# Kernel optimization log

Measured on AMD Instinct MI355X. Metric: run time of the kernel, lower is better.

The kernel has to match this reference:

```python
import jax, jax.numpy as jnp
import numpy as np

B, N, C, H, MLP = 4, 1024, 768, 6, 2304  # num_heads = C // 128
D = C // H  # head dim = 128


def setup_inputs() -> dict:
    key = jax.random.key(0)
    ks = iter(jax.random.split(key, 64))
    def nrm(shape, s=0.02):
        return jax.random.normal(next(ks), shape, jnp.float32) * s
    inp = {}
    for nm in ("queries", "change_emb", "imageA_emb", "imageB_emb", "pe"):
        inp[nm] = jax.random.normal(next(ks), (B, N, C), jnp.float32)
    # three Attention modules: self-attn (1), change->ABC cross (2), imageAB->change cross (3)
    for i in (1, 2, 3):
        for p in ("q", "k", "v", "o"):
            inp[f"w{p}{i}"] = nrm((C, C))       # stored [in, out]; y = x @ W + b
            inp[f"b{p}{i}"] = jnp.zeros((C,), jnp.float32)
    for i in (1, 2, 3):
        inp[f"ln{i}_w"] = jnp.ones((C,), jnp.float32)
        inp[f"ln{i}_b"] = jnp.zeros((C,), jnp.float32)
    inp["mlp_w1"] = nrm((C, MLP)); inp["mlp_b1"] = jnp.zeros((MLP,), jnp.float32)
    inp["mlp_w2"] = nrm((MLP, C)); inp["mlp_b2"] = jnp.zeros((C,), jnp.float32)
    inp["flag_a"] = nrm((C,)); inp["flag_b"] = nrm((C,)); inp["flag_c"] = nrm((C,))
    return inp


def _ln(x, w, b, eps=1e-5):
    m = jnp.mean(x, -1, keepdims=True)
    v = jnp.var(x, -1, keepdims=True)
    return (x - m) * jax.lax.rsqrt(v + eps) * w + b


def _mha(q, k, v, wq, bq, wk, bk, wv, bv, wo, bo):
    b, nq, _ = q.shape
    qh = (q @ wq + bq).reshape(b, nq, H, D)
    kh = (k @ wk + bk).reshape(b, k.shape[1], H, D)
    vh = (v @ wv + bv).reshape(b, v.shape[1], H, D)
    scores = jnp.einsum('bqhd,bkhd->bhqk', qh, kh) / np.float32(np.sqrt(D))
    attn = jax.nn.softmax(scores, axis=-1)
    out = jnp.einsum('bhqk,bkhd->bqhd', attn, vh).reshape(b, nq, H * D)
    return out @ wo + bo


def reference(queries, change_emb, imageA_emb, imageB_emb, pe,
              wq1, bq1, wk1, bk1, wv1, bv1, wo1, bo1,
              wq2, bq2, wk2, bk2, wv2, bv2, wo2, bo2,
              wq3, bq3, wk3, bk3, wv3, bv3, wo3, bo3,
              ln1_w, ln1_b, ln2_w, ln2_b, ln3_w, ln3_b,
              mlp_w1, mlp_b1, mlp_w2, mlp_b2,
              flag_a, flag_b, flag_c):
    # --- self attention on change queries (skip_first_layer_add=False) ---
    q0 = queries + change_emb
    a = _mha(q0 + pe, q0 + pe, q0, wq1, bq1, wk1, bk1, wv1, bv1, wo1, bo1)
    q1 = _ln(q0 + a, ln1_w, ln1_b)
    # --- cross attention: change -> [imageA, imageB, change] ---
    qf = q1 + pe + flag_c
    k2 = jnp.concatenate((imageA_emb + pe + flag_a,
                          imageB_emb + pe + flag_b,
                          q1 + pe + flag_c), axis=1)
    v2 = jnp.concatenate((imageA_emb, imageB_emb, q1), axis=1)
    a = _mha(qf, k2, v2, wq2, bq2, wk2, bk2, wv2, bv2, wo2, bo2)
    q2 = _ln(q1 + a, ln2_w, ln2_b)
    # --- MLP (exact GELU, as nn.GELU default) ---
    mlp_out = jax.nn.gelu(q2 @ mlp_w1 + mlp_b1, approximate=False) @ mlp_w2 + mlp_b2
    q3 = _ln(q2 + mlp_out, ln3_w, ln3_b)
    change_out = q3
    # --- cross attention: [imageA; imageB] -> [image; change], batched along dim 0 ---
    qa = imageA_emb + pe + flag_a
    qb = imageB_emb + pe + flag_b
    ka = jnp.concatenate((imageA_emb + pe + flag_a, q3 + pe + flag_c), axis=1)
    kb = jnp.concatenate((imageB_emb + pe + flag_b, q3 + pe + flag_c), axis=1)
    va = jnp.concatenate((imageA_emb, q3), axis=1)
    vb = jnp.concatenate((imageB_emb, q3), axis=1)
    q = jnp.concatenate((qa, qb), axis=0)   # [2B, N, C]
    k = jnp.concatenate((ka, kb), axis=0)   # [2B, 2N, C]
    v = jnp.concatenate((va, vb), axis=0)
    a = _mha(q, k, v, wq3, bq3, wk3, bk3, wv3, bv3, wo3, bo3)
    q = q + a
    image_A_refined, image_B_refined = jnp.split(q, 2, axis=0)
    return (image_A_refined, image_B_refined, change_out)
```

## Files before the change

### kernel.cpp

```cpp
#include <hip/hip_runtime.h>
#include <hip/hip_bf16.h>
#include <math.h>

typedef short bf16x8 __attribute__((ext_vector_type(8)));
typedef float f32x4 __attribute__((ext_vector_type(4)));
using bf16_t = __hip_bfloat16;

#define DEV static __device__ __forceinline__

DEV unsigned short f2bu(float x) {
  bf16_t h = __float2bfloat16(x);
  unsigned short u;
  __builtin_memcpy(&u, &h, 2);
  return u;
}
DEV void st4(bf16_t* p, float a, float b, float c, float d) {
  ushort4 u;
  u.x = f2bu(a); u.y = f2bu(b); u.z = f2bu(c); u.w = f2bu(d);
  *reinterpret_cast<ushort4*>(p) = u;
}

DEV void async_copy16(const bf16_t* g, bf16_t* lds) {
  __builtin_amdgcn_global_load_lds(
      (const __attribute__((address_space(1))) unsigned int*)g,
      (__attribute__((address_space(3))) unsigned int*)lds, 16, 0, 0);
}

struct WPack {
  const float* s[12];
  bf16_t* d[12];
  float scale0;
};

__global__ __launch_bounds__(256) void k_wt12(WPack pk) {
  __shared__ float tile[32][33];
  int z = blockIdx.z;
  const float* W = pk.s[z];
  bf16_t* WT = pk.d[z];
  float scale = (z == 0) ? pk.scale0 : 1.0f;
  int i0 = blockIdx.x * 32;
  int o0 = blockIdx.y * 32;
  int tx = threadIdx.x & 31, ty = threadIdx.x >> 5;
  for (int r = ty; r < 32; r += 8)
    tile[r][tx] = W[(size_t)(i0 + r) * 768 + (o0 + tx)];
  __syncthreads();
  for (int r = ty; r < 32; r += 8)
    WT[(size_t)(o0 + r) * 768 + (i0 + tx)] = __float2bfloat16(tile[tx][r] * scale);
}

__global__ __launch_bounds__(256) void k_wt(const float* __restrict__ W, bf16_t* __restrict__ WT,
                                            int in_dim, int out_dim) {
  __shared__ float tile[32][33];
  int i0 = blockIdx.x * 32;
  int o0 = blockIdx.y * 32;
  int tx = threadIdx.x & 31, ty = threadIdx.x >> 5;
  for (int r = ty; r < 32; r += 8)
    tile[r][tx] = W[(size_t)(i0 + r) * out_dim + (o0 + tx)];
  __syncthreads();
  for (int r = ty; r < 32; r += 8)
    WT[(size_t)(o0 + r) * in_dim + (i0 + tx)] = __float2bfloat16(tile[tx][r]);
}

__global__ __launch_bounds__(256) void k_bqk(const float* __restrict__ bq, const float* __restrict__ bk,
                                             float* __restrict__ out, float qa) {
  int i = blockIdx.x * 256 + threadIdx.x;
  if (i < 768) out[i] = bq[i] * qa;
  else if (i < 1536) out[i] = bk[i - 768];
}

__global__ __launch_bounds__(256) void k_prep1(const float4* __restrict__ q, const float4* __restrict__ ce,
                                               const float4* __restrict__ pe,
                                               bf16_t* __restrict__ qpe_b, bf16_t* __restrict__ q0_b, int n4) {
  int i = blockIdx.x * 256 + threadIdx.x;
  if (i >= n4) return;
  float4 a = q[i], b = ce[i], p = pe[i];
  float sx = a.x + b.x, sy = a.y + b.y, sz = a.z + b.z, sw = a.w + b.w;
  st4(q0_b + 4 * (size_t)i, sx, sy, sz, sw);
  st4(qpe_b + 4 * (size_t)i, sx + p.x, sy + p.y, sz + p.z, sw + p.w);
}

__global__ __launch_bounds__(256) void k_addpe(const float* __restrict__ x, const float* __restrict__ pe,
                                               const float* __restrict__ flag, bf16_t* __restrict__ out) {
  int idx = blockIdx.x * 256 + threadIdx.x;
  int c = (idx % 192) * 4;
  size_t tok = (size_t)idx * 4;
  float4 xv = *(const float4*)(x + tok);
  float4 p = *(const float4*)(pe + tok);
  float4 f = *(const float4*)(flag + c);
  st4(out + tok, xv.x + p.x + f.x, xv.y + p.y + f.y, xv.z + p.z + f.z, xv.w + p.w + f.w);
}

__global__ __launch_bounds__(256) void k_buildqq(const float* __restrict__ imA, const float* __restrict__ imB,
                                                 const float* __restrict__ pe, const float* __restrict__ fa,
                                                 const float* __restrict__ fb, bf16_t* __restrict__ qq) {
  int idx = blockIdx.x * 256 + threadIdx.x;
  int c4 = idx % 192; int rem = idx / 192;
  int n = rem & 1023; int bb = rem >> 10;
  int b = bb & 3, isB = bb >> 2;
  int c = c4 * 4;
  size_t tok = (size_t)(b * 1024 + n) * 768 + c;
  float4 s = *(const float4*)((isB ? imB : imA) + tok);
  float4 p = *(const float4*)(pe + tok);
  float4 f = *(const float4*)((isB ? fb : fa) + c);
  st4(qq + (size_t)rem * 768 + c, s.x + p.x + f.x, s.y + p.y + f.y, s.z + p.z + f.z, s.w + p.w + f.w);
}

__global__ __launch_bounds__(256) void k_build2b(const float* __restrict__ q1,
    const float* __restrict__ imA, const float* __restrict__ imB, const float* __restrict__ pe,
    const float* __restrict__ fa, const float* __restrict__ fb, const float* __restrict__ fc,
    bf16_t* __restrict__ k2, bf16_t* __restrict__ v2, int b0) {
  int idx = blockIdx.x * 256 + threadIdx.x;
  int c4 = idx % 192; int rem = idx / 192;
  int bi = rem / 3072; int r3 = rem - bi * 3072;
  int seg = r3 >> 10; int n = r3 & 1023;
  int b = b0 + bi;
  int c = c4 * 4;
  size_t tok = (size_t)(b * 1024 + n) * 768 + c;
  float4 p = *(const float4*)(pe + tok);
  const float* srcp; const float* flg;
  if (seg == 0)      { srcp = imA + tok; flg = fa; }
  else if (seg == 1) { srcp = imB + tok; flg = fb; }
  else               { srcp = q1 + tok; flg = fc; }
  float4 s = *(const float4*)srcp;
  float4 f = *(const float4*)(flg + c);
  size_t o = (size_t)idx * 4;
  st4(v2 + o, s.x, s.y, s.z, s.w);
  st4(k2 + o, s.x + p.x + f.x, s.y + p.y + f.y, s.z + p.z + f.z, s.w + p.w + f.w);
}

__global__ __launch_bounds__(256) void k_build3b(const float* __restrict__ q3,
    const float* __restrict__ imA, const float* __restrict__ imB, const float* __restrict__ pe,
    const float* __restrict__ fa, const float* __restrict__ fb, const float* __restrict__ fc,
    bf16_t* __restrict__ k3, bf16_t* __restrict__ v3, int bb0) {
  int idx = blockIdx.x * 256 + threadIdx.x;
  int c4 = idx % 192; int rem = idx / 192;
  int bi = rem >> 11; int r2 = rem & 2047;
  int seg = r2 >> 10; int n = r2 & 1023;
  int bb = bb0 + bi;
  int b = bb & 3; int isB = bb >> 2;
  int c = c4 * 4;
  size_t tok = (size_t)(b * 1024 + n) * 768 + c;
  float4 p = *(const float4*)(pe + tok);
  const float* srcp; const float* flg;
  if (seg == 0) { srcp = (isB ? imB : imA) + tok; flg = isB ? fb : fa; }
  else          { srcp = q3 + tok; flg = fc; }
  float4 s = *(const float4*)srcp;
  float4 f = *(const float4*)(flg + c);
  size_t o = (size_t)idx * 4;
  st4(v3 + o, s.x, s.y, s.z, s.w);
  st4(k3 + o, s.x + p.x + f.x, s.y + p.y + f.y, s.z + p.z + f.z, s.w + p.w + f.w);
}

__global__ __launch_bounds__(256, 3) void k_flash(
    const bf16_t* __restrict__ Q, const bf16_t* __restrict__ K,
    const bf16_t* __restrict__ Vt, bf16_t* __restrict__ O,
    int Nk, int H, int ldq, int ldk, long qStrideB, long kStrideB, long oStrideB) {
  const int z = blockIdx.y; const int b = z / H, h = z % H;
  const bf16_t* Qb = Q + (size_t)b * qStrideB + h * 128;
  const bf16_t* Kb = K + (size_t)b * kStrideB + h * 128;
  const bf16_t* Vb = Vt + (size_t)z * 128 * (size_t)Nk;
  bf16_t* Ob = O + (size_t)b * oStrideB + h * 128;
  const int q0 = blockIdx.x * 64;
  const int tid = threadIdx.x, lane = tid & 63, w = tid >> 6;
  const int g = lane >> 4, c = lane & 15;

  __shared__ bf16_t Ks[64][136];
  __shared__ bf16_t Vs[128][72];
  __shared__ bf16_t Ps[64][72];

  bf16x8 qf[4];
#pragma unroll
  for (int kk = 0; kk < 4; kk++)
    qf[kk] = *reinterpret_cast<const bf16x8*>(
        &Qb[(size_t)(q0 + w * 16 + c) * ldq + kk * 32 + g * 8]);

  f32x4 oa[8];
  float m[4], l[4];
#pragma unroll
  for (int d = 0; d < 8; d++) { f32x4 zz = {0.f, 0.f, 0.f, 0.f}; oa[d] = zz; }
#pragma unroll
  for (int r = 0; r < 4; r++) { m[r] = -1.0e30f; l[r] = 0.f; }

  const int kr_ = tid >> 4, kc_ = (tid & 15) * 8;
  const int vr_ = tid >> 3, vc_ = (tid & 7) * 8;

  const int nt = Nk >> 6;
  for (int t = 0; t < nt; ++t) {
    const int k0 = t << 6;
#pragma unroll
    for (int p = 0; p < 4; p++)
      *reinterpret_cast<uint4*>(&Ks[p * 16 + kr_][kc_]) =
          *reinterpret_cast<const uint4*>(&Kb[(size_t)(k0 + p * 16 + kr_) * ldk + kc_]);
#pragma unroll
    for (int p = 0; p < 4; p++)
      *reinterpret_cast<uint4*>(&Vs[p * 32 + vr_][vc_]) =
          *reinterpret_cast<const uint4*>(&Vb[(size_t)(p * 32 + vr_) * Nk + k0 + vc_]);
    __syncthreads();

    f32x4 s[4];
#pragma unroll
    for (int j = 0; j < 4; j++) { f32x4 zz = {0.f, 0.f, 0.f, 0.f}; s[j] = zz; }
    __builtin_amdgcn_s_setprio(1);
#pragma unroll
    for (int kk = 0; kk < 4; kk++)
#pragma unroll
      for (int j = 0; j < 4; j++) {
        bf16x8 kf = *reinterpret_cast<const bf16x8*>(&Ks[j * 16 + c][kk * 32 + g * 8]);
        s[j] = __builtin_amdgcn_mfma_f32_16x16x32_bf16(qf[kk], kf, s[j], 0, 0, 0);
      }
    __builtin_amdgcn_s_setprio(0);

    float tl[4];
#pragma unroll
    for (int r = 0; r < 4; r++)
      tl[r] = fmaxf(fmaxf(s[0][r], s[1][r]), fmaxf(s[2][r], s[3][r]));
    float ex = fmaxf(fmaxf(tl[0] - m[0], tl[1] - m[1]), fmaxf(tl[2] - m[2], tl[3] - m[3]));
    if (__any(ex > 8.0f)) {
#pragma unroll
      for (int r = 0; r < 4; r++) {
        float tv = tl[r];
        tv = fmaxf(tv, __shfl_xor(tv, 1));
        tv = fmaxf(tv, __shfl_xor(tv, 2));
        tv = fmaxf(tv, __shfl_xor(tv, 4));
        tv = fmaxf(tv, __shfl_xor(tv, 8));
        float mn = fmaxf(m[r], tv);
        float f = exp2f(m[r] - mn);
        m[r] = mn;
        l[r] *= f;
#pragma unroll
        for (int d = 0; d < 8; d++) oa[d][r] *= f;
      }
    }
#pragma unroll
    for (int j = 0; j < 4; j++)
#pragma unroll
      for (int r = 0; r < 4; r++) {
        float p = exp2f(s[j][r] - m[r]);
        l[r] += p;
        Ps[w * 16 + g * 4 + r][j * 16 + c] = __float2bfloat16(p);
      }

    __builtin_amdgcn_s_setprio(1);
#pragma unroll
    for (int kk = 0; kk < 2; kk++) {
      bf16x8 pf = *reinterpret_cast<const bf16x8*>(&Ps[w * 16 + c][kk * 32 + g * 8]);
#pragma unroll
      for (int d = 0; d < 8; d++) {
        bf16x8 vf = *reinterpret_cast<const bf16x8*>(&Vs[d * 16 + c][kk * 32 + g * 8]);
        oa[d] = __builtin_amdgcn_mfma_f32_16x16x32_bf16(pf, vf, oa[d], 0, 0, 0);
      }
    }
    __builtin_amdgcn_s_setprio(0);
    __syncthreads();
  }

  float inv[4];
#pragma unroll
  for (int r = 0; r < 4; r++) {
    float t2 = l[r];
    t2 += __shfl_xor(t2, 1);
    t2 += __shfl_xor(t2, 2);
    t2 += __shfl_xor(t2, 4);
    t2 += __shfl_xor(t2, 8);
    inv[r] = 1.0f / t2;
  }
#pragma unroll
  for (int d = 0; d < 8; d++) {
    int col = d * 16 + c;
#pragma unroll
    for (int r = 0; r < 4; r++) {
      int row = q0 + w * 16 + g * 4 + r;
      Ob[(size_t)row * 768 + col] = __float2bfloat16(oa[d][r] * inv[r]);
    }
  }
}

__global__ __launch_bounds__(256) void k_ln(const float* __restrict__ X1, const float* __restrict__ X2,
                                            const float* __restrict__ A,
                                            const float* __restrict__ w, const float* __restrict__ bvec,
                                            float* __restrict__ outf, bf16_t* __restrict__ outb) {
  int row = blockIdx.x, tid = threadIdx.x;
  size_t base = (size_t)row * 768;
  float v0 = X1[base + tid] + A[base + tid];
  float v1 = X1[base + tid + 256] + A[base + tid + 256];
  float v2 = X1[base + tid + 512] + A[base + tid + 512];
  if (X2) {
    v0 += X2[base + tid]; v1 += X2[base + tid + 256]; v2 += X2[base + tid + 512];
  }
  float s = v0 + v1 + v2;
  for (int o = 32; o; o >>= 1) s += __shfl_xor(s, o);
  __shared__ float sm[8];
  int wv = tid >> 6, ln = tid & 63;
  if (ln == 0) sm[wv] = s;
  __syncthreads();
  s = sm[0] + sm[1] + sm[2] + sm[3];
  float mean = s * (1.0f / 768.0f);
  float d0 = v0 - mean, d1 = v1 - mean, d2 = v2 - mean;
  float ss = d0 * d0 + d1 * d1 + d2 * d2;
  for (int o = 32; o; o >>= 1) ss += __shfl_xor(ss, o);
  if (ln == 0) sm[4 + wv] = ss;
  __syncthreads();
  ss = sm[4] + sm[5] + sm[6] + sm[7];
  float rstd = rsqrtf(ss * (1.0f / 768.0f) + 1e-5f);
  float o0 = d0 * rstd * w[tid] + bvec[tid];
  float o1 = d1 * rstd * w[tid + 256] + bvec[tid + 256];
  float o2 = d2 * rstd * w[tid + 512] + bvec[tid + 512];
  outf[base + tid] = o0; outf[base + tid + 256] = o1; outf[base + tid + 512] = o2;
  if (outb) {
    outb[base + tid] = __float2bfloat16(o0);
    outb[base + tid + 256] = __float2bfloat16(o1);
    outb[base + tid + 512] = __float2bfloat16(o2);
  }
}

__global__ __launch_bounds__(256) void k_out3f(const float* __restrict__ imA, const float* __restrict__ imB,
                                               const float* __restrict__ pe, const float* __restrict__ fa,
                                               const float* __restrict__ fb, float* __restrict__ out) {
  int idx = blockIdx.x * 256 + threadIdx.x;
  int c4 = idx % 192; int rem = idx / 192;
  int n = rem & 1023; int bb = rem >> 10;
  int b = bb & 3, isB = bb >> 2;
  int c = c4 * 4;
  size_t tok = (size_t)(b * 1024 + n) * 768 + c;
  float4 sv = *(const float4*)((isB ? imB : imA) + tok);
  float4 p = *(const float4*)(pe + tok);
  float4 f = *(const float4*)((isB ? fb : fa) + c);
  size_t o = (size_t)idx * 4;
  float4 cur = *(float4*)(out + o);
  cur.x += sv.x + p.x + f.x;
  cur.y += sv.y + p.y + f.y;
  cur.z += sv.z + p.z + f.z;
  cur.w += sv.w + p.w + f.w;
  *(float4*)(out + o) = cur;
}

template<int OUTBF, int GELU, int OUTVT>
__global__ __launch_bounds__(256, 2) void k_gemm(
    const bf16_t* __restrict__ X, const bf16_t* __restrict__ Wt,
    const float* __restrict__ bias, void* __restrict__ Out,
    int M, int Nout, int K, int ldx, int ldw, int ldo, float alpha, int vNk) {
  const int brow = blockIdx.y * 128;
  const int bcol = blockIdx.x * 128;

  __shared__ bf16_t As[128 * 32];
  __shared__ bf16_t Bs[128 * 32];

  const int tid = threadIdx.x;
  const int lane = tid & 63;
  const int wave = tid >> 6;
  const int wr = wave >> 1;
  const int wc = wave & 1;

  f32x4 acc[4][4];
#pragma unroll
  for (int i = 0; i < 4; i++)
#pragma unroll
    for (int j = 0; j < 4; j++) {
      f32x4 zz = {0.f, 0.f, 0.f, 0.f};
      acc[i][j] = zz;
    }

  const int sr = lane >> 2;
  const int sc = (lane & 3) * 8;
  const int lrow = lane & 15;
  const int kch = (lane >> 4) * 8;

  const int nK = K >> 5;
  for (int kk = 0; kk < nK; ++kk) {
    const int k0 = kk << 5;
#pragma unroll
    for (int q = 0; q < 2; q++) {
      const int rows = wave * 32 + q * 16;
      async_copy16(X + (size_t)(brow + rows + sr) * ldx + k0 + sc, As + rows * 32);
      async_copy16(Wt + (size_t)(bcol + rows + sr) * ldw + k0 + sc, Bs + rows * 32);
    }
    __syncthreads();

    bf16x8 afr[4], bfr[4];
#pragma unroll
    for (int i = 0; i < 4; i++)
      afr[i] = *reinterpret_cast<const bf16x8*>(&As[(wr * 64 + i * 16 + lrow) * 32 + kch]);
#pragma unroll
    for (int j = 0; j < 4; j++)
      bfr[j] = *reinterpret_cast<const bf16x8*>(&Bs[(wc * 64 + j * 16 + lrow) * 32 + kch]);
#pragma unroll
    for (int i = 0; i < 4; i++)
#pragma unroll
      for (int j = 0; j < 4; j++)
        acc[i][j] = __builtin_amdgcn_mfma_f32_16x16x32_bf16(afr[i], bfr[j], acc[i][j], 0, 0, 0);
    __syncthreads();
  }

  const int lcol = lane & 15;
  const int lrow4 = (lane >> 4) * 4;

  if (OUTVT) {
    const int bi = brow / vNk;
    const int n0 = brow - bi * vNk;
#pragma unroll
    for (int i = 0; i < 4; i++) {
      int rloc = n0 + wr * 64 + i * 16 + lrow4;
#pragma unroll
      for (int j = 0; j < 4; j++) {
        int col = bcol + wc * 64 + j * 16 + lcol;
        int hh = col >> 7, dd = col & 127;
        float bv = bias ? bias[col] : 0.0f;
        ushort4 u;
        u.x = f2bu((acc[i][j][0] + bv) * alpha);
        u.y = f2bu((acc[i][j][1] + bv) * alpha);
        u.z = f2bu((acc[i][j][2] + bv) * alpha);
        u.w = f2bu((acc[i][j][3] + bv) * alpha);
        bf16_t* dst = reinterpret_cast<bf16_t*>(Out) +
                      ((size_t)(bi * 6 + hh) * 128 + dd) * (size_t)vNk + rloc;
        *reinterpret_cast<ushort4*>(dst) = u;
      }
    }
    return;
  }

#pragma unroll
  for (int i = 0; i < 4; i++) {
    int row0 = brow + wr * 64 + i * 16 + lrow4;
#pragma unroll
    for (int j = 0; j < 4; j++) {
      int col = bcol + wc * 64 + j * 16 + lcol;
      float bv = bias ? bias[col] : 0.0f;
#pragma unroll
      for (int r = 0; r < 4; r++) {
        float v = (acc[i][j][r] + bv) * alpha;
        if (GELU) v = 0.5f * v * (1.0f + erff(v * 0.70710678118f));
        size_t idx = (size_t)(row0 + r) * ldo + col;
        if (OUTBF) reinterpret_cast<bf16_t*>(Out)[idx] = __float2bfloat16(v);
        else reinterpret_cast<float*>(Out)[idx] = v;
      }
    }
  }
}

struct GArgs {
  const bf16_t* X; const bf16_t* Wt; const float* bias; bf16_t* Out;
  int K, ldx, ldw, ldo, vNk, mode;
};

__global__ __launch_bounds__(256, 2) void k_gemmD(GArgs a0, GArgs a1, int cnt0, int nx0, int nx1) {
  GArgs a; int bx, by;
  {
    int idx = blockIdx.x;
    if (idx < cnt0) { a = a0; bx = idx % nx0; by = idx / nx0; }
    else { idx -= cnt0; a = a1; bx = idx % nx1; by = idx / nx1; }
  }
  const int brow = by * 128;
  const int bcol = bx * 128;

  __shared__ bf16_t As[128 * 32];
  __shared__ bf16_t Bs[128 * 32];

  const int tid = threadIdx.x;
  const int lane = tid & 63;
  const int wave = tid >> 6;
  const int wr = wave >> 1;
  const int wc = wave & 1;

  f32x4 acc[4][4];
#pragma unroll
  for (int i = 0; i < 4; i++)
#pragma unroll
    for (int j = 0; j < 4; j++) {
      f32x4 zz = {0.f, 0.f, 0.f, 0.f};
      acc[i][j] = zz;
    }

  const int sr = lane >> 2;
  const int sc = (lane & 3) * 8;
  const int lrow = lane & 15;
  const int kch = (lane >> 4) * 8;

  const int nK = a.K >> 5;
  for (int kk = 0; kk < nK; ++kk) {
    const int k0 = kk << 5;
#pragma unroll
    for (int q = 0; q < 2; q++) {
      const int rows = wave * 32 + q * 16;
      async_copy16(a.X + (size_t)(brow + rows + sr) * a.ldx + k0 + sc, As + rows * 32);
      async_copy16(a.Wt + (size_t)(bcol + rows + sr) * a.ldw + k0 + sc, Bs + rows * 32);
    }
    __syncthreads();

    bf16x8 afr[4], bfr[4];
#pragma unroll
    for (int i = 0; i < 4; i++)
      afr[i] = *reinterpret_cast<const bf16x8*>(&As[(wr * 64 + i * 16 + lrow) * 32 + kch]);
#pragma unroll
    for (int j = 0; j < 4; j++)
      bfr[j] = *reinterpret_cast<const bf16x8*>(&Bs[(wc * 64 + j * 16 + lrow) * 32 + kch]);
#pragma unroll
    for (int i = 0; i < 4; i++)
#pragma unroll
      for (int j = 0; j < 4; j++)
        acc[i][j] = __builtin_amdgcn_mfma_f32_16x16x32_bf16(afr[i], bfr[j], acc[i][j], 0, 0, 0);
    __syncthreads();
  }

  const int lcol = lane & 15;
  const int lrow4 = (lane >> 4) * 4;

  if (a.mode == 2) {
    const int bi = brow / a.vNk;
    const int n0 = brow - bi * a.vNk;
#pragma unroll
    for (int i = 0; i < 4; i++) {
      int rloc = n0 + wr * 64 + i * 16 + lrow4;
#pragma unroll
      for (int j = 0; j < 4; j++) {
        int col = bcol + wc * 64 + j * 16 + lcol;
        int hh = col >> 7, dd = col & 127;
        float bv = a.bias[col];
        ushort4 u;
        u.x = f2bu(acc[i][j][0] + bv);
        u.y = f2bu(acc[i][j][1] + bv);
        u.z = f2bu(acc[i][j][2] + bv);
        u.w = f2bu(acc[i][j][3] + bv);
        bf16_t* dst = a.Out + ((size_t)(bi * 6 + hh) * 128 + dd) * (size_t)a.vNk + rloc;
        *reinterpret_cast<ushort4*>(dst) = u;
      }
    }
  } else {
#pragma unroll
    for (int i = 0; i < 4; i++) {
      int row0 = brow + wr * 64 + i * 16 + lrow4;
#pragma unroll
      for (int j = 0; j < 4; j++) {
        int col = bcol + wc * 64 + j * 16 + lcol;
        float bv = a.bias[col];
#pragma unroll
        for (int r = 0; r < 4; r++)
          a.Out[(size_t)(row0 + r) * a.ldo + col] = __float2bfloat16(acc[i][j][r] + bv);
      }
    }
  }
}

static inline void gemm(hipStream_t st, const bf16_t* X, const bf16_t* Wt, const float* bias,
                        void* out, int outBf, int gelu, int M, int N, int K,
                        int ldx, int ldw, int ldo, float alpha = 1.0f, int vtNk = 0) {
  dim3 g(N / 128, M / 128), blk(256);
  if (vtNk) {
    k_gemm<1, 0, 1><<<g, blk, 0, st>>>(X, Wt, bias, out, M, N, K, ldx, ldw, ldo, alpha, vtNk);
  } else if (outBf) {
    if (gelu) k_gemm<1, 1, 0><<<g, blk, 0, st>>>(X, Wt, bias, out, M, N, K, ldx, ldw, ldo, alpha, 0);
    else      k_gemm<1, 0, 0><<<g, blk, 0, st>>>(X, Wt, bias, out, M, N, K, ldx, ldw, ldo, alpha, 0);
  } else      k_gemm<0, 0, 0><<<g, blk, 0, st>>>(X, Wt, bias, out, M, N, K, ldx, ldw, ldo, alpha, 0);
}

static inline void gemm_pair(hipStream_t st, GArgs a0, int M0, int N0, GArgs a1, int M1, int N1) {
  int nx0 = N0 / 128, ny0 = M0 / 128;
  int nx1 = N1 / 128, ny1 = M1 / 128;
  int cnt0 = nx0 * ny0, cnt1 = nx1 * ny1;
  k_gemmD<<<dim3(cnt0 + cnt1), 256, 0, st>>>(a0, a1, cnt0, nx0, nx1);
}

extern "C" void kernel_launch(void* const* d_in, const int* in_sizes, int n_in,
                              void* d_out, int out_size, void* d_ws, size_t ws_size,
                              hipStream_t stream) {
  (void)in_sizes; (void)n_in; (void)out_size;
  constexpr int B = 4, N = 1024, C = 768, Hh = 6, MLPD = 2304;
  constexpr size_t BNC = (size_t)B * N * C;
  constexpr size_t NC  = (size_t)N * C;
  const float scale = 0.08838834764831845f;
  const float qalpha = scale * 1.4426950408889634f;

  const float* queries = (const float*)d_in[0];
  const float* change  = (const float*)d_in[1];
  const float* imA     = (const float*)d_in[2];
  const float* imB     = (const float*)d_in[3];
  const float* pe      = (const float*)d_in[4];
  const float* bq1 = (const float*)d_in[6];  const float* bk1 = (const float*)d_in[8];
  const float* bv1 = (const float*)d_in[10]; const float* bo1 = (const float*)d_in[12];
  const float* bq2 = (const float*)d_in[14]; const float* bk2 = (const float*)d_in[16];
  const float* bv2 = (const float*)d_in[18]; const float* bo2 = (const float*)d_in[20];
  const float* bq3 = (const float*)d_in[22]; const float* bk3 = (const float*)d_in[24];
  const float* bv3 = (const float*)d_in[26]; const float* bo3 = (const float*)d_in[28];
  const float* ln1w = (const float*)d_in[29]; const float* ln1b = (const float*)d_in[30];
  const float* ln2w = (const float*)d_in[31]; const float* ln2b = (const float*)d_in[32];
  const float* ln3w = (const float*)d_in[33]; const float* ln3b = (const float*)d_in[34];
  const float* mb1 = (const float*)d_in[36]; const float* mb2 = (const float*)d_in[38];
  const float* fa = (const float*)d_in[39];
  const float* fb = (const float*)d_in[40];
  const float* fc = (const float*)d_in[41];

  char* base = (char*)d_ws;
  size_t off = 0;
  auto alloc = [&](size_t bytes) -> void* {
    void* p = base + off;
    off += (bytes + 255) & ~(size_t)255;
    return p;
  };

  bf16_t* WT[14];
  const int widx[14] = {5, 7, 9, 11, 13, 15, 17, 19, 21, 23, 25, 27, 35, 37};
  const int wins[14] = {768, 768, 768, 768, 768, 768, 768, 768, 768, 768, 768, 768, 768, 2304};
  const int wout[14] = {768, 768, 768, 768, 768, 768, 768, 768, 768, 768, 768, 768, 2304, 768};
  for (int i = 0; i < 14; i++) WT[i] = (bf16_t*)alloc((size_t)wins[i] * wout[i] * 2);
  float* bqk1 = (float*)alloc(1536 * 4);
  float*  q1  = (float*)alloc(BNC * 4);
  float*  q2  = (float*)alloc(BNC * 4);
  bf16_t* q2b = (bf16_t*)alloc(BNC * 2);
  const size_t arena = off;

  const size_t slack = 4u << 20;
  size_t rem = (ws_size > arena + slack) ? ws_size - arena - slack : 0;
  int g2 = 4;
  while (g2 > 1 && 3 * BNC * 2 + (size_t)g2 * 4 * (3 * NC * 2) > rem) g2 >>= 1;
  int h3 = 8;
  while (h3 > 1 && 3 * (2 * BNC) * 2 + (size_t)h3 * 4 * (2 * NC * 2) > rem) h3 >>= 1;

  float* dof = (float*)d_out;
  float* chg = dof + 2 * BNC;

  WPack pk;
  for (int i = 0; i < 12; i++) { pk.s[i] = (const float*)d_in[widx[i]]; pk.d[i] = WT[i]; }
  pk.scale0 = qalpha;
  k_wt12<<<dim3(24, 24, 12), 256, 0, stream>>>(pk);
  k_wt<<<dim3(24, 72), 256, 0, stream>>>((const float*)d_in[35], WT[12], 768, 2304);
  k_wt<<<dim3(72, 24), 256, 0, stream>>>((const float*)d_in[37], WT[13], 2304, 768);
  k_bqk<<<dim3(6), 256, 0, stream>>>(bq1, bk1, bqk1, qalpha);

  off = arena;
  bf16_t* qpe_b = (bf16_t*)alloc(BNC * 2);
  bf16_t* q0_b  = (bf16_t*)alloc(BNC * 2);
  bf16_t* QKh   = (bf16_t*)alloc((size_t)B * N * 1536 * 2);
  bf16_t* vT1   = (bf16_t*)alloc(BNC * 2);
  bf16_t* attC  = (bf16_t*)alloc(BNC * 2);
  float*  a1    = dof;

  k_prep1<<<dim3((int)(BNC / 4 / 256)), 256, 0, stream>>>(
      (const float4*)queries, (const float4*)change, (const float4*)pe, qpe_b, q0_b, (int)(BNC / 4));
  {
    GArgs aqk = {qpe_b, WT[0], bqk1, QKh, C, C, C, 1536, 0, 1};
    GArgs av  = {q0_b,  WT[2], bv1,  vT1, C, C, C, 0,  N, 2};
    gemm_pair(stream, aqk, B * N, 1536, av, B * N, C);
  }
  k_flash<<<dim3(N / 64, B * Hh), 256, 0, stream>>>(QKh, QKh + 768, vT1, attC,
                                                    N, Hh, 1536, 1536,
                                                    (long)N * 1536, (long)N * 1536, (long)NC);
  gemm(stream, attC, WT[3], bo1, a1, 0, 0, B * N, C, C, C, C, C);
  k_ln<<<dim3(B * N), 256, 0, stream>>>(queries, change, a1, ln1w, ln1b, q1, (bf16_t*)nullptr);

  off = arena;
  bf16_t* qf    = (bf16_t*)alloc(BNC * 2);
  bf16_t* Q2h   = (bf16_t*)alloc(BNC * 2);
  bf16_t* attC2 = (bf16_t*)alloc(BNC * 2);
  bf16_t* k2in  = (bf16_t*)alloc((size_t)g2 * 3 * NC * 2);
  bf16_t* v2in  = (bf16_t*)alloc((size_t)g2 * 3 * NC * 2);
  bf16_t* K2h   = (bf16_t*)alloc((size_t)g2 * 3 * NC * 2);
  bf16_t* vT2   = (bf16_t*)alloc((size_t)g2 * 3 * NC * 2);
  float*  a2    = dof;

  k_addpe<<<dim3((int)(BNC / 4 / 256)), 256, 0, stream>>>(q1, pe, fc, qf);
  gemm(stream, qf, WT[4], bq2, Q2h, 1, 0, B * N, C, C, C, C, C, qalpha);
  for (int b0 = 0; b0 < B; b0 += g2) {
    const int Nk = 3 * N;
    k_build2b<<<dim3((int)((size_t)g2 * 3 * NC / 4 / 256)), 256, 0, stream>>>(
        q1, imA, imB, pe, fa, fb, fc, k2in, v2in, b0);
    {
      GArgs ak = {k2in, WT[5], bk2, K2h, C, C, C, C, 0, 1};
      GArgs av = {v2in, WT[6], bv2, vT2, C, C, C, 0, Nk, 2};
      gemm_pair(stream, ak, g2 * Nk, C, av, g2 * Nk, C);
    }
    k_flash<<<dim3(N / 64, g2 * Hh), 256, 0, stream>>>(Q2h + (size_t)b0 * NC, K2h, vT2,
                                                       attC2 + (size_t)b0 * NC, Nk, Hh, C, C,
                                                       (long)NC, (long)(3 * NC), (long)NC);
  }
  gemm(stream, attC2, WT[7], bo2, a2, 0, 0, B * N, C, C, C, C, C);
  k_ln<<<dim3(B * N), 256, 0, stream>>>(q1, (const float*)nullptr, a2, ln2w, ln2b, q2, q2b);

  off = arena;
  bf16_t* h1 = (bf16_t*)alloc((size_t)B * N * MLPD * 2);
  float*  a3 = dof;
  gemm(stream, q2b, WT[12], mb1, h1, 1, 1, B * N, MLPD, C, C, C, MLPD);
  gemm(stream, h1, WT[13], mb2, a3, 0, 0, B * N, C, MLPD, MLPD, MLPD, C);
  k_ln<<<dim3(B * N), 256, 0, stream>>>(q2, (const float*)nullptr, a3, ln3w, ln3b, chg, (bf16_t*)nullptr);

  off = arena;
  bf16_t* qq    = (bf16_t*)alloc(2 * BNC * 2);
  bf16_t* Q3h   = (bf16_t*)alloc(2 * BNC * 2);
  bf16_t* attC3 = (bf16_t*)alloc(2 * BNC * 2);
  bf16_t* k3in  = (bf16_t*)alloc((size_t)h3 * 2 * NC * 2);
  bf16_t* v3in  = (bf16_t*)alloc((size_t)h3 * 2 * NC * 2);
  bf16_t* K3h   = (bf16_t*)alloc((size_t)h3 * 2 * NC * 2);
  bf16_t* vT3   = (bf16_t*)alloc((size_t)h3 * 2 * NC * 2);

  k_buildqq<<<dim3((int)(2 * BNC / 4 / 256)), 256, 0, stream>>>(imA, imB, pe, fa, fb, qq);
  gemm(stream, qq, WT[8], bq3, Q3h, 1, 0, 2 * B * N, C, C, C, C, C, qalpha);
  for (int bb0 = 0; bb0 < 2 * B; bb0 += h3) {
    const int Nk = 2 * N;
    k_build3b<<<dim3((int)((size_t)h3 * 2 * NC / 4 / 256)), 256, 0, stream>>>(
        chg, imA, imB, pe, fa, fb, fc, k3in, v3in, bb0);
    {
      GArgs ak = {k3in, WT[9],  bk3, K3h, C, C, C, C, 0, 1};
      GArgs av = {v3in, WT[10], bv3, vT3, C, C, C, 0, Nk, 2};
      gemm_pair(stream, ak, h3 * Nk, C, av, h3 * Nk, C);
    }
    k_flash<<<dim3(N / 64, h3 * Hh), 256, 0, stream>>>(Q3h + (size_t)bb0 * NC, K3h, vT3,
                                                       attC3 + (size_t)bb0 * NC, Nk, Hh, C, C,
                                                       (long)NC, (long)(2 * NC), (long)NC);
  }
  gemm(stream, attC3, WT[11], bo3, dof, 0, 0, 2 * B * N, C, C, C, C, C);
  k_out3f<<<dim3((int)(2 * BNC / 4 / 256)), 256, 0, stream>>>(imA, imB, pe, fa, fb, dof);
}
```

Measured before the change: 728.1 us.

## Batch Q projections into grouped GEMM launches and fuse output residual

Generalizes the dual-GEMM kernel to take three problems. The stage-3 Q projection now runs alongside the stage-1 QKV launch, and the stage-2 Q projection is batched with the K/V projections. The final output projection adds the residual inside the GEMM epilogue, reading the bf16 qq buffer, which replaces the separate k_out3f pass. This cuts kernel launches and a full fp32 read-modify-write, but the residual is now taken from bf16 (qq) rather than fp32 inputs, which loses some precision.

```diff
diff --git a/kernel.cpp b/kernel.cpp
--- a/kernel.cpp
+++ b/kernel.cpp
@@ -313,141 +313,21 @@
   }
 }
 
-__global__ __launch_bounds__(256) void k_out3f(const float* __restrict__ imA, const float* __restrict__ imB,
-                                               const float* __restrict__ pe, const float* __restrict__ fa,
-                                               const float* __restrict__ fb, float* __restrict__ out) {
-  int idx = blockIdx.x * 256 + threadIdx.x;
-  int c4 = idx % 192; int rem = idx / 192;
-  int n = rem & 1023; int bb = rem >> 10;
-  int b = bb & 3, isB = bb >> 2;
-  int c = c4 * 4;
-  size_t tok = (size_t)(b * 1024 + n) * 768 + c;
-  float4 sv = *(const float4*)((isB ? imB : imA) + tok);
-  float4 p = *(const float4*)(pe + tok);
-  float4 f = *(const float4*)((isB ? fb : fa) + c);
-  size_t o = (size_t)idx * 4;
-  float4 cur = *(float4*)(out + o);
-  cur.x += sv.x + p.x + f.x;
-  cur.y += sv.y + p.y + f.y;
-  cur.z += sv.z + p.z + f.z;
-  cur.w += sv.w + p.w + f.w;
-  *(float4*)(out + o) = cur;
-}
-
-template<int OUTBF, int GELU, int OUTVT>
-__global__ __launch_bounds__(256, 2) void k_gemm(
-    const bf16_t* __restrict__ X, const bf16_t* __restrict__ Wt,
-    const float* __restrict__ bias, void* __restrict__ Out,
-    int M, int Nout, int K, int ldx, int ldw, int ldo, float alpha, int vNk) {
-  const int brow = blockIdx.y * 128;
-  const int bcol = blockIdx.x * 128;
-
-  __shared__ bf16_t As[128 * 32];
-  __shared__ bf16_t Bs[128 * 32];
-
-  const int tid = threadIdx.x;
-  const int lane = tid & 63;
-  const int wave = tid >> 6;
-  const int wr = wave >> 1;
-  const int wc = wave & 1;
-
-  f32x4 acc[4][4];
-#pragma unroll
-  for (int i = 0; i < 4; i++)
-#pragma unroll
-    for (int j = 0; j < 4; j++) {
-      f32x4 zz = {0.f, 0.f, 0.f, 0.f};
-      acc[i][j] = zz;
-    }
-
-  const int sr = lane >> 2;
-  const int sc = (lane & 3) * 8;
-  const int lrow = lane & 15;
-  const int kch = (lane >> 4) * 8;
-
-  const int nK = K >> 5;
-  for (int kk = 0; kk < nK; ++kk) {
-    const int k0 = kk << 5;
-#pragma unroll
-    for (int q = 0; q < 2; q++) {
-      const int rows = wave * 32 + q * 16;
-      async_copy16(X + (size_t)(brow + rows + sr) * ldx + k0 + sc, As + rows * 32);
-      async_copy16(Wt + (size_t)(bcol + rows + sr) * ldw + k0 + sc, Bs + rows * 32);
-    }
-    __syncthreads();
-
-    bf16x8 afr[4], bfr[4];
-#pragma unroll
-    for (int i = 0; i < 4; i++)
-      afr[i] = *reinterpret_cast<const bf16x8*>(&As[(wr * 64 + i * 16 + lrow) * 32 + kch]);
-#pragma unroll
-    for (int j = 0; j < 4; j++)
-      bfr[j] = *reinterpret_cast<const bf16x8*>(&Bs[(wc * 64 + j * 16 + lrow) * 32 + kch]);
-#pragma unroll
-    for (int i = 0; i < 4; i++)
-#pragma unroll
-      for (int j = 0; j < 4; j++)
-        acc[i][j] = __builtin_amdgcn_mfma_f32_16x16x32_bf16(afr[i], bfr[j], acc[i][j], 0, 0, 0);
-    __syncthreads();
-  }
-
-  const int lcol = lane & 15;
-  const int lrow4 = (lane >> 4) * 4;
-
-  if (OUTVT) {
-    const int bi = brow / vNk;
-    const int n0 = brow - bi * vNk;
-#pragma unroll
-    for (int i = 0; i < 4; i++) {
-      int rloc = n0 + wr * 64 + i * 16 + lrow4;
-#pragma unroll
-      for (int j = 0; j < 4; j++) {
-        int col = bcol + wc * 64 + j * 16 + lcol;
-        int hh = col >> 7, dd = col & 127;
-        float bv = bias ? bias[col] : 0.0f;
-        ushort4 u;
-        u.x = f2bu((acc[i][j][0] + bv) * alpha);
-        u.y = f2bu((acc[i][j][1] + bv) * alpha);
-        u.z = f2bu((acc[i][j][2] + bv) * alpha);
-        u.w = f2bu((acc[i][j][3] + bv) * alpha);
-        bf16_t* dst = reinterpret_cast<bf16_t*>(Out) +
-                      ((size_t)(bi * 6 + hh) * 128 + dd) * (size_t)vNk + rloc;
-        *reinterpret_cast<ushort4*>(dst) = u;
-      }
-    }
-    return;
-  }
-
-#pragma unroll
-  for (int i = 0; i < 4; i++) {
-    int row0 = brow + wr * 64 + i * 16 + lrow4;
-#pragma unroll
-    for (int j = 0; j < 4; j++) {
-      int col = bcol + wc * 64 + j * 16 + lcol;
-      float bv = bias ? bias[col] : 0.0f;
-#pragma unroll
-      for (int r = 0; r < 4; r++) {
-        float v = (acc[i][j][r] + bv) * alpha;
-        if (GELU) v = 0.5f * v * (1.0f + erff(v * 0.70710678118f));
-        size_t idx = (size_t)(row0 + r) * ldo + col;
-        if (OUTBF) reinterpret_cast<bf16_t*>(Out)[idx] = __float2bfloat16(v);
-        else reinterpret_cast<float*>(Out)[idx] = v;
-      }
-    }
-  }
-}
-
 struct GArgs {
-  const bf16_t* X; const bf16_t* Wt; const float* bias; bf16_t* Out;
+  const bf16_t* X; const bf16_t* Wt; const float* bias; void* Out;
+  const bf16_t* resid;
   int K, ldx, ldw, ldo, vNk, mode;
+  float alpha;
 };
 
-__global__ __launch_bounds__(256, 2) void k_gemmD(GArgs a0, GArgs a1, int cnt0, int nx0, int nx1) {
+__global__ __launch_bounds__(256, 2) void k_gemmM(GArgs a0, GArgs a1, GArgs a2,
+                                                  int c0, int c01, int nx0, int nx1, int nx2) {
   GArgs a; int bx, by;
   {
     int idx = blockIdx.x;
-    if (idx < cnt0) { a = a0; bx = idx % nx0; by = idx / nx0; }
-    else { idx -= cnt0; a = a1; bx = idx % nx1; by = idx / nx1; }
+    if (idx < c0) { a = a0; bx = idx % nx0; by = idx / nx0; }
+    else if (idx < c01) { idx -= c0; a = a1; bx = idx % nx1; by = idx / nx1; }
+    else { idx -= c01; a = a2; bx = idx % nx2; by = idx / nx2; }
   }
   const int brow = by * 128;
   const int bcol = bx * 128;
@@ -520,11 +400,12 @@
         u.y = f2bu(acc[i][j][1] + bv);
         u.z = f2bu(acc[i][j][2] + bv);
         u.w = f2bu(acc[i][j][3] + bv);
-        bf16_t* dst = a.Out + ((size_t)(bi * 6 + hh) * 128 + dd) * (size_t)a.vNk + rloc;
+        bf16_t* dst = reinterpret_cast<bf16_t*>(a.Out) +
+                      ((size_t)(bi * 6 + hh) * 128 + dd) * (size_t)a.vNk + rloc;
         *reinterpret_cast<ushort4*>(dst) = u;
       }
     }
-  } else {
+  } else if (a.mode == 3) {
 #pragma unroll
     for (int i = 0; i < 4; i++) {
       int row0 = brow + wr * 64 + i * 16 + lrow4;
@@ -533,8 +414,111 @@
         int col = bcol + wc * 64 + j * 16 + lcol;
         float bv = a.bias[col];
 #pragma unroll
+        for (int r = 0; r < 4; r++) {
+          size_t idx = (size_t)(row0 + r) * a.ldo + col;
+          float rv = __bfloat162float(a.resid[(size_t)(row0 + r) * 768 + col]);
+          reinterpret_cast<float*>(a.Out)[idx] = acc[i][j][r] + bv + rv;
+        }
+      }
+    }
+  } else {
+#pragma unroll
+    for (int i = 0; i < 4; i++) {
+      int row0 = brow + wr * 64 + i * 16 + lrow4;
+#pragma unroll
+      for (int j = 0; j < 4; j++) {
+        int col = bcol + wc * 64 + j * 16 + lcol;
+        float bv = a.bias[col];
+#pragma unroll
         for (int r = 0; r < 4; r++)
-          a.Out[(size_t)(row0 + r) * a.ldo + col] = __float2bfloat16(acc[i][j][r] + bv);
+          reinterpret_cast<bf16_t*>(a.Out)[(size_t)(row0 + r) * a.ldo + col] =
+              __float2bfloat16((acc[i][j][r] + bv) * a.alpha);
+      }
+    }
+  }
+}
+
+static inline void gemmM3(hipStream_t st, GArgs a0, int M0, int N0,
+                          GArgs a1, int M1, int N1, GArgs a2, int M2, int N2) {
+  int nx0 = N0 / 128, nx1 = N1 / 128, nx2 = N2 > 0 ? N2 / 128 : 1;
+  int c0 = nx0 * (M0 / 128), c1 = nx1 * (M1 / 128), c2 = nx2 * (M2 / 128);
+  k_gemmM<<<dim3(c0 + c1 + c2), 256, 0, st>>>(a0, a1, a2, c0, c0 + c1, nx0, nx1, nx2);
+}
+
+template<int OUTBF, int GELU>
+__global__ __launch_bounds__(256, 2) void k_gemm(
+    const bf16_t* __restrict__ X, const bf16_t* __restrict__ Wt,
+    const float* __restrict__ bias, void* __restrict__ Out,
+    int M, int Nout, int K, int ldx, int ldw, int ldo, float alpha) {
+  const int brow = blockIdx.y * 128;
+  const int bcol = blockIdx.x * 128;
+
+  __shared__ bf16_t As[128 * 32];
+  __shared__ bf16_t Bs[128 * 32];
+
+  const int tid = threadIdx.x;
+  const int lane = tid & 63;
+  const int wave = tid >> 6;
+  const int wr = wave >> 1;
+  const int wc = wave & 1;
+
+  f32x4 acc[4][4];
+#pragma unroll
+  for (int i = 0; i < 4; i++)
+#pragma unroll
+    for (int j = 0; j < 4; j++) {
+      f32x4 zz = {0.f, 0.f, 0.f, 0.f};
+      acc[i][j] = zz;
+    }
+
+  const int sr = lane >> 2;
+  const int sc = (lane & 3) * 8;
+  const int lrow = lane & 15;
+  const int kch = (lane >> 4) * 8;
+
+  const int nK = K >> 5;
+  for (int kk = 0; kk < nK; ++kk) {
+    const int k0 = kk << 5;
+#pragma unroll
+    for (int q = 0; q < 2; q++) {
+      const int rows = wave * 32 + q * 16;
+      async_copy16(X + (size_t)(brow + rows + sr) * ldx + k0 + sc, As + rows * 32);
+      async_copy16(Wt + (size_t)(bcol + rows + sr) * ldw + k0 + sc, Bs + rows * 32);
+    }
+    __syncthreads();
+
+    bf16x8 afr[4], bfr[4];
+#pragma unroll
+    for (int i = 0; i < 4; i++)
+      afr[i] = *reinterpret_cast<const bf16x8*>(&As[(wr * 64 + i * 16 + lrow) * 32 + kch]);
+#pragma unroll
+    for (int j = 0; j < 4; j++)
+      bfr[j] = *reinterpret_cast<const bf16x8*>(&Bs[(wc * 64 + j * 16 + lrow) * 32 + kch]);
+#pragma unroll
+    for (int i = 0; i < 4; i++)
+#pragma unroll
+      for (int j = 0; j < 4; j++)
+        acc[i][j] = __builtin_amdgcn_mfma_f32_16x16x32_bf16(afr[i], bfr[j], acc[i][j], 0, 0, 0);
+    __syncthreads();
+  }
+
+  const int lcol = lane & 15;
+  const int lrow4 = (lane >> 4) * 4;
+
+#pragma unroll
+  for (int i = 0; i < 4; i++) {
+    int row0 = brow + wr * 64 + i * 16 + lrow4;
+#pragma unroll
+    for (int j = 0; j < 4; j++) {
+      int col = bcol + wc * 64 + j * 16 + lcol;
+      float bv = bias ? bias[col] : 0.0f;
+#pragma unroll
+      for (int r = 0; r < 4; r++) {
+        float v = (acc[i][j][r] + bv) * alpha;
+        if (GELU) v = 0.5f * v * (1.0f + erff(v * 0.70710678118f));
+        size_t idx = (size_t)(row0 + r) * ldo + col;
+        if (OUTBF) reinterpret_cast<bf16_t*>(Out)[idx] = __float2bfloat16(v);
+        else reinterpret_cast<float*>(Out)[idx] = v;
       }
     }
   }
@@ -542,21 +526,12 @@
 
 static inline void gemm(hipStream_t st, const bf16_t* X, const bf16_t* Wt, const float* bias,
                         void* out, int outBf, int gelu, int M, int N, int K,
-                        int ldx, int ldw, int ldo, float alpha = 1.0f, int vtNk = 0) {
+                        int ldx, int ldw, int ldo, float alpha = 1.0f) {
   dim3 g(N / 128, M / 128), blk(256);
-  if (vtNk) {
-    k_gemm<1, 0, 1><<<g, blk, 0, st>>>(X, Wt, bias, out, M, N, K, ldx, ldw, ldo, alpha, vtNk);
-  } else if (outBf) {
-    if (gelu) k_gemm<1, 1, 0><<<g, blk, 0, st>>>(X, Wt, bias, out, M, N, K, ldx, ldw, ldo, alpha, 0);
-    else      k_gemm<1, 0, 0><<<g, blk, 0, st>>>(X, Wt, bias, out, M, N, K, ldx, ldw, ldo, alpha, 0);
-  } else      k_gemm<0, 0, 0><<<g, blk, 0, st>>>(X, Wt, bias, out, M, N, K, ldx, ldw, ldo, alpha, 0);
-}
-
-static inline void gemm_pair(hipStream_t st, GArgs a0, int M0, int N0, GArgs a1, int M1, int N1) {
-  int nx0 = N0 / 128, ny0 = M0 / 128;
-  int nx1 = N1 / 128, ny1 = M1 / 128;
-  int cnt0 = nx0 * ny0, cnt1 = nx1 * ny1;
-  k_gemmD<<<dim3(cnt0 + cnt1), 256, 0, st>>>(a0, a1, cnt0, nx0, nx1);
+  if (outBf) {
+    if (gelu) k_gemm<1, 1><<<g, blk, 0, st>>>(X, Wt, bias, out, M, N, K, ldx, ldw, ldo, alpha);
+    else      k_gemm<1, 0><<<g, blk, 0, st>>>(X, Wt, bias, out, M, N, K, ldx, ldw, ldo, alpha);
+  } else      k_gemm<0, 0><<<g, blk, 0, st>>>(X, Wt, bias, out, M, N, K, ldx, ldw, ldo, alpha);
 }
 
 extern "C" void kernel_launch(void* const* d_in, const int* in_sizes, int n_in,
@@ -605,6 +580,8 @@
   float*  q1  = (float*)alloc(BNC * 4);
   float*  q2  = (float*)alloc(BNC * 4);
   bf16_t* q2b = (bf16_t*)alloc(BNC * 2);
+  bf16_t* qq    = (bf16_t*)alloc(2 * BNC * 2);
+  bf16_t* Q3h   = (bf16_t*)alloc(2 * BNC * 2);
   const size_t arena = off;
 
   const size_t slack = 4u << 20;
@@ -612,7 +589,7 @@
   int g2 = 4;
   while (g2 > 1 && 3 * BNC * 2 + (size_t)g2 * 4 * (3 * NC * 2) > rem) g2 >>= 1;
   int h3 = 8;
-  while (h3 > 1 && 3 * (2 * BNC) * 2 + (size_t)h3 * 4 * (2 * NC * 2) > rem) h3 >>= 1;
+  while (h3 > 1 && BNC * 2 + (size_t)h3 * 4 * (2 * NC * 2) > rem) h3 >>= 1;
 
   float* dof = (float*)d_out;
   float* chg = dof + 2 * BNC;
@@ -635,10 +612,12 @@
 
   k_prep1<<<dim3((int)(BNC / 4 / 256)), 256, 0, stream>>>(
       (const float4*)queries, (const float4*)change, (const float4*)pe, qpe_b, q0_b, (int)(BNC / 4));
+  k_buildqq<<<dim3((int)(2 * BNC / 4 / 256)), 256, 0, stream>>>(imA, imB, pe, fa, fb, qq);
   {
-    GArgs aqk = {qpe_b, WT[0], bqk1, QKh, C, C, C, 1536, 0, 1};
-    GArgs av  = {q0_b,  WT[2], bv1,  vT1, C, C, C, 0,  N, 2};
-    gemm_pair(stream, aqk, B * N, 1536, av, B * N, C);
+    GArgs aqk = {qpe_b, WT[0], bqk1, QKh, nullptr, C, C, C, 1536, 0, 1, 1.0f};
+    GArgs av  = {q0_b,  WT[2], bv1,  vT1, nullptr, C, C, C, 0,  N, 2, 1.0f};
+    GArgs aq3 = {qq,    WT[8], bq3,  Q3h, nullptr, C, C, C, C,  0, 1, qalpha};
+    gemmM3(stream, aqk, B * N, 1536, av, B * N, C, aq3, 2 * B * N, C);
   }
   k_flash<<<dim3(N / 64, B * Hh), 256, 0, stream>>>(QKh, QKh + 768, vT1, attC,
                                                     N, Hh, 1536, 1536,
@@ -657,19 +636,29 @@
   float*  a2    = dof;
 
   k_addpe<<<dim3((int)(BNC / 4 / 256)), 256, 0, stream>>>(q1, pe, fc, qf);
-  gemm(stream, qf, WT[4], bq2, Q2h, 1, 0, B * N, C, C, C, C, C, qalpha);
-  for (int b0 = 0; b0 < B; b0 += g2) {
+  if (g2 == 4) {
     const int Nk = 3 * N;
-    k_build2b<<<dim3((int)((size_t)g2 * 3 * NC / 4 / 256)), 256, 0, stream>>>(
-        q1, imA, imB, pe, fa, fb, fc, k2in, v2in, b0);
-    {
-      GArgs ak = {k2in, WT[5], bk2, K2h, C, C, C, C, 0, 1};
-      GArgs av = {v2in, WT[6], bv2, vT2, C, C, C, 0, Nk, 2};
-      gemm_pair(stream, ak, g2 * Nk, C, av, g2 * Nk, C);
-    }
-    k_flash<<<dim3(N / 64, g2 * Hh), 256, 0, stream>>>(Q2h + (size_t)b0 * NC, K2h, vT2,
-                                                       attC2 + (size_t)b0 * NC, Nk, Hh, C, C,
-                                                       (long)NC, (long)(3 * NC), (long)NC);
+    k_build2b<<<dim3((int)((size_t)4 * 3 * NC / 4 / 256)), 256, 0, stream>>>(
+        q1, imA, imB, pe, fa, fb, fc, k2in, v2in, 0);
+    GArgs aq = {qf,   WT[4], bq2, Q2h, nullptr, C, C, C, C, 0, 1, qalpha};
+    GArgs ak = {k2in, WT[5], bk2, K2h, nullptr, C, C, C, C, 0, 1, 1.0f};
+    GArgs av = {v2in, WT[6], bv2, vT2, nullptr, C, C, C, 0, Nk, 2, 1.0f};
+    gemmM3(stream, aq, B * N, C, ak, 4 * Nk, C, av, 4 * Nk, C);
+    k_flash<<<dim3(N / 64, 4 * Hh), 256, 0, stream>>>(Q2h, K2h, vT2, attC2, Nk, Hh, C, C,
+                                                      (long)NC, (long)(3 * NC), (long)NC);
+  } else {
+    gemm(stream, qf, WT[4], bq2, Q2h, 1, 0, B * N, C, C, C, C, C, qalpha);
+    for (int b0 = 0; b0 < B; b0 += g2) {
+      const int Nk = 3 * N;
+      k_build2b<<<dim3((int)((size_t)g2 * 3 * NC / 4 / 256)), 256, 0, stream>>>(
+          q1, imA, imB, pe, fa, fb, fc, k2in, v2in, b0);
+      GArgs ak = {k2in, WT[5], bk2, K2h, nullptr, C, C, C, C, 0, 1, 1.0f};
+      GArgs av = {v2in, WT[6], bv2, vT2, nullptr, C, C, C, 0, Nk, 2, 1.0f};
+      gemmM3(stream, ak, g2 * Nk, C, av, g2 * Nk, C, av, 0, 128);
+      k_flash<<<dim3(N / 64, g2 * Hh), 256, 0, stream>>>(Q2h + (size_t)b0 * NC, K2h, vT2,
+                                                         attC2 + (size_t)b0 * NC, Nk, Hh, C, C,
+                                                         (long)NC, (long)(3 * NC), (long)NC);
+    }
   }
   gemm(stream, attC2, WT[7], bo2, a2, 0, 0, B * N, C, C, C, C, C);
   k_ln<<<dim3(B * N), 256, 0, stream>>>(q1, (const float*)nullptr, a2, ln2w, ln2b, q2, q2b);
@@ -682,29 +671,25 @@
   k_ln<<<dim3(B * N), 256, 0, stream>>>(q2, (const float*)nullptr, a3, ln3w, ln3b, chg, (bf16_t*)nullptr);
 
   off = arena;
-  bf16_t* qq    = (bf16_t*)alloc(2 * BNC * 2);
-  bf16_t* Q3h   = (bf16_t*)alloc(2 * BNC * 2);
   bf16_t* attC3 = (bf16_t*)alloc(2 * BNC * 2);
   bf16_t* k3in  = (bf16_t*)alloc((size_t)h3 * 2 * NC * 2);
   bf16_t* v3in  = (bf16_t*)alloc((size_t)h3 * 2 * NC * 2);
   bf16_t* K3h   = (bf16_t*)alloc((size_t)h3 * 2 * NC * 2);
   bf16_t* vT3   = (bf16_t*)alloc((size_t)h3 * 2 * NC * 2);
 
-  k_buildqq<<<dim3((int)(2 * BNC / 4 / 256)), 256, 0, stream>>>(imA, imB, pe, fa, fb, qq);
-  gemm(stream, qq, WT[8], bq3, Q3h, 1, 0, 2 * B * N, C, C, C, C, C, qalpha);
   for (int bb0 = 0; bb0 < 2 * B; bb0 += h3) {
     const int Nk = 2 * N;
     k_build3b<<<dim3((int)((size_t)h3 * 2 * NC / 4 / 256)), 256, 0, stream>>>(
         chg, imA, imB, pe, fa, fb, fc, k3in, v3in, bb0);
-    {
-      GArgs ak = {k3in, WT[9],  bk3, K3h, C, C, C, C, 0, 1};
-      GArgs av = {v3in, WT[10], bv3, vT3, C, C, C, 0, Nk, 2};
-      gemm_pair(stream, ak, h3 * Nk, C, av, h3 * Nk, C);
-    }
+    GArgs ak = {k3in, WT[9],  bk3, K3h, nullptr, C, C, C, C, 0, 1, 1.0f};
+    GArgs av = {v3in, WT[10], bv3, vT3, nullptr, C, C, C, 0, Nk, 2, 1.0f};
+    gemmM3(stream, ak, h3 * Nk, C, av, h3 * Nk, C, av, 0, 128);
     k_flash<<<dim3(N / 64, h3 * Hh), 256, 0, stream>>>(Q3h + (size_t)bb0 * NC, K3h, vT3,
                                                        attC3 + (size_t)bb0 * NC, Nk, Hh, C, C,
                                                        (long)NC, (long)(2 * NC), (long)NC);
   }
-  gemm(stream, attC3, WT[11], bo3, dof, 0, 0, 2 * B * N, C, C, C, C, C);
-  k_out3f<<<dim3((int)(2 * BNC / 4 / 256)), 256, 0, stream>>>(imA, imB, pe, fa, fb, dof);
-}
+  {
+    GArgs ao = {attC3, WT[11], bo3, dof, qq, C, C, C, C, 0, 3, 1.0f};
+    gemmM3(stream, ao, 2 * B * N, C, ao, 0, 128, ao, 0, 128);
+  }
+}
```

After: 692.9 us. 4.8% less time.
